# Kernel optimization log

Measured on AMD Instinct MI355X. Metric: run time of the kernel, lower is better.

Reference implementation:

```python
import jax, jax.numpy as jnp
import numpy as np

N = 50000   # nodes
E = 800000  # edges (avg degree 16)
DIMS = [(128, 128), (128, 128), (128, 64)]  # (in, out) per SAGEConv layer
EPS_BN = 1e-5
EPS_NORM = 1e-12


def _make_layer(key, din, dout):
    k1, k2 = jax.random.split(key)
    s = 1.0 / np.sqrt(din)
    return (
        jax.random.normal(k1, (dout, din), jnp.float32) * s,  # Wl: neighbor linear
        jnp.zeros((dout,), jnp.float32),                      # bl
        jax.random.normal(k2, (dout, din), jnp.float32) * s,  # Wr: root linear (no bias in PyG)
        jnp.ones((dout,), jnp.float32),                       # bn gamma
        jnp.zeros((dout,), jnp.float32),                      # bn beta
        jnp.zeros((dout,), jnp.float32),                      # bn running mean
        jnp.ones((dout,), jnp.float32),                       # bn running var
    )


def setup_inputs() -> dict:
    key = jax.random.key(0)
    kx, ke, k0, k1, k2 = jax.random.split(key, 5)
    inp = {
        "x": jax.random.normal(kx, (N, 128), jnp.float32),
        "edge_index": jax.random.randint(ke, (2, E), 0, N, dtype=jnp.int32),
    }
    for i, (k, (din, dout)) in enumerate(zip([k0, k1, k2], DIMS)):
        Wl, bl, Wr, g, b, rm, rv = _make_layer(k, din, dout)
        inp.update({f"Wl{i}": Wl, f"bl{i}": bl, f"Wr{i}": Wr,
                    f"g{i}": g, f"b{i}": b, f"rm{i}": rm, f"rv{i}": rv})
    return inp


def _sage_conv(x, src, dst, Wl, bl, Wr):
    # mean aggregation of incoming messages: gather src features, scatter-add at dst
    agg = jax.ops.segment_sum(x[src], dst, num_segments=N)          # [N, din]
    deg = jax.ops.segment_sum(jnp.ones((src.shape[0],), x.dtype), dst, num_segments=N)
    mean = agg / jnp.maximum(deg, 1.0)[:, None]
    return mean @ Wl.T + bl + x @ Wr.T


def _bn_eval(x, g, b, rm, rv):
    return g * (x - rm) * jax.lax.rsqrt(rv + EPS_BN) + b


def reference(x, edge_index,
              Wl0, bl0, Wr0, g0, b0, rm0, rv0,
              Wl1, bl1, Wr1, g1, b1, rm1, rv1,
              Wl2, bl2, Wr2, g2, b2, rm2, rv2):
    src, dst = edge_index[0], edge_index[1]
    layers = [
        (Wl0, bl0, Wr0, g0, b0, rm0, rv0),
        (Wl1, bl1, Wr1, g1, b1, rm1, rv1),
        (Wl2, bl2, Wr2, g2, b2, rm2, rv2),
    ]
    h = x
    for i, (Wl, bl, Wr, g, b, rm, rv) in enumerate(layers):
        h = _bn_eval(_sage_conv(h, src, dst, Wl, bl, Wr), g, b, rm, rv)
        if i < len(layers) - 1:
            h = jax.nn.relu(h)  # dropout is identity in eval mode
    # F.normalize(p=2, dim=1)
    return h / jnp.maximum(jnp.linalg.norm(h, axis=1, keepdims=True), EPS_NORM)
```

## Files before the change

### kernel.cpp

```cpp
#include <hip/hip_runtime.h>
#include <hip/hip_bf16.h>

#define CDIV(a,b) (((a)+(b)-1)/(b))
#define NBUCK_MAX 512
#define AGG_CAP  1536
#define AGGF_CAP 3072

typedef __attribute__((ext_vector_type(8))) short short8;
typedef __attribute__((ext_vector_type(4))) float f32x4;
typedef __attribute__((ext_vector_type(2))) float f32x2;

static __device__ __forceinline__ unsigned short f2bf(float f){
  union { float f; unsigned u; } v; v.f = f;
  unsigned r = v.u + 0x7fffu + ((v.u >> 16) & 1u);
  return (unsigned short)(r >> 16);
}
static __device__ __forceinline__ unsigned pack2(float lo, float hi){
  return (unsigned)f2bf(lo) | ((unsigned)f2bf(hi) << 16);
}
static __device__ __forceinline__ float bf2f(unsigned short s){
  union { unsigned u; float f; } v; v.u = ((unsigned)s) << 16; return v.f;
}
static __device__ __forceinline__ unsigned pk_fp8x4(float a, float b, float c, float d){
  int v = __builtin_amdgcn_cvt_pk_fp8_f32(a, b, 0, false);
  v = __builtin_amdgcn_cvt_pk_fp8_f32(c, d, v, true);
  return (unsigned)v;
}

#define ACCQ16(v) { f32x2 q0 = __builtin_amdgcn_cvt_pk_f32_fp8((int)v.x, false); \
                    f32x2 q1 = __builtin_amdgcn_cvt_pk_f32_fp8((int)v.x, true);  \
                    f32x2 q2 = __builtin_amdgcn_cvt_pk_f32_fp8((int)v.y, false); \
                    f32x2 q3 = __builtin_amdgcn_cvt_pk_f32_fp8((int)v.y, true);  \
                    f32x2 q4 = __builtin_amdgcn_cvt_pk_f32_fp8((int)v.z, false); \
                    f32x2 q5 = __builtin_amdgcn_cvt_pk_f32_fp8((int)v.z, true);  \
                    f32x2 q6 = __builtin_amdgcn_cvt_pk_f32_fp8((int)v.w, false); \
                    f32x2 q7 = __builtin_amdgcn_cvt_pk_f32_fp8((int)v.w, true);  \
                    a0 += q0.x; a1 += q0.y; a2  += q1.x; a3  += q1.y; \
                    a4 += q2.x; a5 += q2.y; a6  += q3.x; a7  += q3.y; \
                    a8 += q4.x; a9 += q4.y; a10 += q5.x; a11 += q5.y; \
                    a12 += q6.x; a13 += q6.y; a14 += q7.x; a15 += q7.y; }


struct WtpArgs {
  const float *W0, *W1, *bl, *g, *b, *rm, *rv;
  unsigned short* Bpk; float *sc; float *sh;
  int kblk, dout, do_bn, nblk, perm;
};

static __device__ __forceinline__ void wtp_one(const WtpArgs& a, int idx){
  int NB16 = a.kblk*32*a.dout;
  if (idx < NB16){
    int j = idx & 7, lane = (idx >> 3) & 63, rest = idx >> 9;
    int NT = a.dout >> 4;
    int nt = rest % NT, kk = rest / NT;
    int nn = nt*16 + (lane & 15);
    int k  = kk*32 + ((lane >> 4) * 8) + j;
    float v;
    if (k < 128){
      int kc = a.perm ? (((k & 7) << 4) | (k >> 3)) : k;
      v = a.W0[nn*128 + kc];
    } else {
      v = a.W1[nn*128 + (k - 128)];
    }
    a.Bpk[idx] = f2bf(v);
  } else if (a.do_bn && idx < NB16 + a.dout){
    int jj = idx - NB16;
    float s = a.g[jj] * rsqrtf(a.rv[jj] + 1e-5f);
    a.sc[jj] = s;
    a.sh[jj] = (a.bl[jj] - a.rm[jj]) * s + a.b[jj];
  }
}


__global__ __launch_bounds__(256) void k_prep(const float* __restrict__ x, int n4, unsigned* __restrict__ xb,
                                              unsigned* __restrict__ xq,
                                              const int* __restrict__ dst, int E,
                                              int* __restrict__ bcnt, int nbuck,
                                              int castBlocks, int histBlocks,
                                              WtpArgs a0, WtpArgs a1, WtpArgs a2, WtpArgs a3){
  __shared__ int s[NBUCK_MAX];
  int b = blockIdx.x, t = threadIdx.x;
  if (b < castBlocks){
    int i = b*256 + t;
    if (i < n4){
      float4 v = ((const float4*)x)[i];
      uint2 o; o.x = pack2(v.x, v.y); o.y = pack2(v.z, v.w);
      ((uint2*)xb)[i] = o;
      xq[i] = pk_fp8x4(v.x, v.y, v.z, v.w);
    }
    return;
  }
  b -= castBlocks;
  if (b < histBlocks){
    for (int i=t;i<nbuck;i+=256) s[i] = 0;
    __syncthreads();
    constexpr int EPT = 16;
    int e0 = b*256*EPT;
    #pragma unroll
    for (int i=0;i<EPT;i++){
      int e = e0 + i*256 + t;
      if (e < E) atomicAdd(&s[dst[e] >> 7], 1);
    }
    __syncthreads();
    for (int i=t;i<nbuck;i+=256){
      int c = s[i];
      if (c > 0) atomicAdd(&bcnt[i], c);
    }
    return;
  }
  b -= histBlocks;
  if (b < a0.nblk){ wtp_one(a0, b*256 + t); return; }
  b -= a0.nblk;
  if (b < a1.nblk){ wtp_one(a1, b*256 + t); return; }
  b -= a1.nblk;
  if (b < a2.nblk){ wtp_one(a2, b*256 + t); return; }
  b -= a2.nblk;
  wtp_one(a3, b*256 + t);
}

__global__ __launch_bounds__(256) void k_bscan(const int* __restrict__ bcnt, int nbuck,
                                               int* __restrict__ bbase){
  __shared__ int s[256];
  int t = threadIdx.x;
  int a0 = (2*t   < nbuck) ? bcnt[2*t]   : 0;
  int a1 = (2*t+1 < nbuck) ? bcnt[2*t+1] : 0;
  s[t] = a0 + a1; __syncthreads();
  for (int d=1; d<256; d<<=1){
    int u = (t>=d) ? s[t-d] : 0;
    __syncthreads();
    s[t] += u;
    __syncthreads();
  }
  int excl = s[t] - (a0 + a1);
  if (2*t   < nbuck) bbase[2*t]   = excl;
  if (2*t+1 < nbuck) bbase[2*t+1] = excl + a0;
  if (t == 255) bbase[nbuck] = s[255];
}

__global__ __launch_bounds__(256) void k_bucketA(const int* __restrict__ src, const int* __restrict__ dst,
                                                 int E, const int* __restrict__ bbase,
                                                 int* __restrict__ bcur, unsigned* __restrict__ ebuf, int nbuck){
  __shared__ int scnt[NBUCK_MAX];
  __shared__ int sbase[NBUCK_MAX];
  __shared__ int sboff[NBUCK_MAX];
  int t = threadIdx.x;
  for (int i=t;i<nbuck;i+=256) scnt[i] = 0;
  __syncthreads();
  constexpr int EPT = 16;
  int e0 = blockIdx.x*256*EPT;
  int b[EPT]; unsigned pk[EPT];
  #pragma unroll
  for (int i=0;i<EPT;i++){
    int e = e0 + i*256 + t;
    if (e < E){
      int d = dst[e];
      b[i] = d >> 7;
      pk[i] = ((unsigned)(d & 127) << 16) | (unsigned)src[e];
      atomicAdd(&scnt[b[i]], 1);
    } else b[i] = -1;
  }
  __syncthreads();
  for (int i=t;i<nbuck;i+=256){
    int c = scnt[i];
    sbase[i] = (c > 0) ? atomicAdd(&bcur[i], c) : 0;
    sboff[i] = bbase[i];
    scnt[i] = 0;
  }
  __syncthreads();
  #pragma unroll
  for (int i=0;i<EPT;i++){
    if (b[i] >= 0){
      int p = atomicAdd(&scnt[b[i]], 1);
      ebuf[(size_t)sboff[b[i]] + sbase[b[i]] + p] = pk[i];
    }
  }
}

__global__ __launch_bounds__(256) void k_bucketB(const unsigned* __restrict__ ebuf, const int* __restrict__ bbase,
                                                 int N, int* __restrict__ off, int* __restrict__ csr){
  int b = blockIdx.x;
  int n0 = b << 7, n1 = min(n0 + 128, N);
  __shared__ int sdeg[128];
  __shared__ int sabs[129];
  __shared__ int cur[128];
  int t = threadIdx.x;
  if (t < 128){ sdeg[t] = 0; cur[t] = 0; }
  __syncthreads();
  int e0 = bbase[b], e1 = bbase[b+1];
  for (int e = e0 + t; e < e1; e += 256)
    atomicAdd(&sdeg[ebuf[e] >> 16], 1);
  __syncthreads();
  for (int d=1; d<128; d<<=1){
    int u = (t < 128 && t >= d) ? sdeg[t-d] : 0;
    __syncthreads();
    if (t < 128) sdeg[t] += u;
    __syncthreads();
  }
  if (t == 0) sabs[0] = e0;
  if (t < 128) sabs[t+1] = e0 + sdeg[t];
  __syncthreads();
  if (t <= n1 - n0) off[n0 + t] = sabs[t];
  for (int e = e0 + t; e < e1; e += 256){
    unsigned pr = ebuf[e];
    int ln = (int)(pr >> 16);
    int p = atomicAdd(&cur[ln], 1);
    csr[sabs[ln] + p] = (int)(pr & 0xffffu);
  }
}


__global__ __launch_bounds__(256) void k_agg(const uint4* __restrict__ hq4, const int* __restrict__ off,
                                             const int* __restrict__ csr, int n, uint4* __restrict__ mean4){
  __shared__ int scsr[AGG_CAP];
  __shared__ int sw[2];
  int t = threadIdx.x;
  int nodeblk = blockIdx.x * 32;
  if (t < 2) sw[t] = off[min(nodeblk + t*32, n)];
  __syncthreads();
  int e0b = sw[0];
  int span = sw[1] - e0b;
  for (int i = t; i < span && i < AGG_CAP; i += 256) scsr[i] = csr[e0b + i];
  __syncthreads();

  int lane = t & 63;
  int sl = lane & 7;
  int node = nodeblk + (t >> 3);
  bool valid = node < n;
  int s0 = valid ? off[node]   : 0;
  int s1 = valid ? off[node+1] : 0;
  float a0=0,a1=0,a2=0,a3=0,a4=0,a5=0,a6=0,a7=0;
  float a8=0,a9=0,a10=0,a11=0,a12=0,a13=0,a14=0,a15=0;
  int e = s0;
  for (; e + 8 <= s1; e += 8){
    int le = e - e0b;
    int i0,i1,i2,i3,i4,i5,i6,i7;
    if (le + 8 <= AGG_CAP){
      i0 = scsr[le];   i1 = scsr[le+1]; i2 = scsr[le+2]; i3 = scsr[le+3];
      i4 = scsr[le+4]; i5 = scsr[le+5]; i6 = scsr[le+6]; i7 = scsr[le+7];
    } else {
      i0 = csr[e];   i1 = csr[e+1]; i2 = csr[e+2]; i3 = csr[e+3];
      i4 = csr[e+4]; i5 = csr[e+5]; i6 = csr[e+6]; i7 = csr[e+7];
    }
    uint4 v0 = hq4[(size_t)i0*8 + sl];
    uint4 v1 = hq4[(size_t)i1*8 + sl];
    uint4 v2 = hq4[(size_t)i2*8 + sl];
    uint4 v3 = hq4[(size_t)i3*8 + sl];
    uint4 v4 = hq4[(size_t)i4*8 + sl];
    uint4 v5 = hq4[(size_t)i5*8 + sl];
    uint4 v6 = hq4[(size_t)i6*8 + sl];
    uint4 v7 = hq4[(size_t)i7*8 + sl];
    ACCQ16(v0); ACCQ16(v1); ACCQ16(v2); ACCQ16(v3);
    ACCQ16(v4); ACCQ16(v5); ACCQ16(v6); ACCQ16(v7);
  }
  for (; e + 4 <= s1; e += 4){
    int le = e - e0b;
    int i0,i1,i2,i3;
    if (le + 4 <= AGG_CAP){
      i0 = scsr[le]; i1 = scsr[le+1]; i2 = scsr[le+2]; i3 = scsr[le+3];
    } else {
      i0 = csr[e]; i1 = csr[e+1]; i2 = csr[e+2]; i3 = csr[e+3];
    }
    uint4 v0 = hq4[(size_t)i0*8 + sl];
    uint4 v1 = hq4[(size_t)i1*8 + sl];
    uint4 v2 = hq4[(size_t)i2*8 + sl];
    uint4 v3 = hq4[(size_t)i3*8 + sl];
    ACCQ16(v0); ACCQ16(v1); ACCQ16(v2); ACCQ16(v3);
  }
  for (; e < s1; e++){
    int le = e - e0b;
    int ii = (le < AGG_CAP) ? scsr[le] : csr[e];
    uint4 v = hq4[(size_t)ii*8 + sl];
    ACCQ16(v);
  }
  if (valid){
    int d = s1 - s0;
    float inv = 1.0f / (float)(d > 0 ? d : 1);
    uint4 o0, o1;
    o0.x = pack2(a0*inv,  a1*inv);  o0.y = pack2(a2*inv,  a3*inv);
    o0.z = pack2(a4*inv,  a5*inv);  o0.w = pack2(a6*inv,  a7*inv);
    o1.x = pack2(a8*inv,  a9*inv);  o1.y = pack2(a10*inv, a11*inv);
    o1.z = pack2(a12*inv, a13*inv); o1.w = pack2(a14*inv, a15*inv);
    size_t base = (size_t)node*16 + (size_t)sl*2;
    mean4[base]   = o0;
    mean4[base+1] = o1;
  }
}


template<bool YL>
__global__ __launch_bounds__(256, 2) void k_gemm_hid(
    const unsigned short* __restrict__ A0, const unsigned short* __restrict__ A1,
    const unsigned short* __restrict__ Bpk, const float* __restrict__ sc,
    const float* __restrict__ sh, const unsigned short* __restrict__ BpkL,
    unsigned short* __restrict__ outh, unsigned* __restrict__ outq,
    unsigned* __restrict__ outyl, int n){
  __shared__ unsigned short Bs[256*128];
  int t = threadIdx.x;
  {
    const uint4* s = (const uint4*)Bpk;
    uint4* d = (uint4*)Bs;
    #pragma unroll
    for (int i=0;i<16;i++) d[i*256 + t] = s[i*256 + t];
  }
  __syncthreads();

  int lane = t & 63, w = t >> 6;
  int quad = lane >> 4, c = lane & 15;
  int mb = blockIdx.x*128, woff = w*32;
  int r0 = mb + woff + c;
  int r1 = r0 + 16;

  f32x4 acc[2][8];
  #pragma unroll
  for (int mt=0;mt<2;mt++)
    #pragma unroll
    for (int nt=0;nt<8;nt++) acc[mt][nt] = (f32x4){0.f,0.f,0.f,0.f};

  #pragma unroll
  for (int kk=0; kk<8; kk++){
    const unsigned short* ab = (kk >= 4) ? A1 : A0;
    int ka = (kk & 3)*32 + quad*8;
    short8 a0 = {0,0,0,0,0,0,0,0}, a1 = {0,0,0,0,0,0,0,0};
    if (r0 < n) a0 = *(const short8*)(ab + (size_t)r0*128 + ka);
    if (r1 < n) a1 = *(const short8*)(ab + (size_t)r1*128 + ka);
    #pragma unroll
    for (int nt=0; nt<8; nt++){
      short8 b = *(const short8*)&Bs[(size_t)((kk*8 + nt)*64 + lane)*8];
      acc[0][nt] = __builtin_amdgcn_mfma_f32_16x16x32_bf16(a0, b, acc[0][nt], 0, 0, 0);
      acc[1][nt] = __builtin_amdgcn_mfma_f32_16x16x32_bf16(a1, b, acc[1][nt], 0, 0, 0);
    }
  }

  float scv[8], shv[8];
  #pragma unroll
  for (int nt=0;nt<8;nt++){ scv[nt] = sc[nt*16 + c]; shv[nt] = sh[nt*16 + c]; }

  #pragma unroll
  for (int mt=0; mt<2; mt++){
    #pragma unroll
    for (int r=0;r<4;r++){
      int row = mb + woff + mt*16 + quad*4 + r;
      if (row < n){
        float u[8];
        #pragma unroll
        for (int nt=0;nt<8;nt++){
          float uu = acc[mt][nt][r]*scv[nt] + shv[nt];
          u[nt] = fmaxf(uu, 0.f);
          outh[(size_t)row*128 + nt*16 + c] = f2bf(u[nt]);
        }
        if constexpr (!YL){
          uint2 q;
          q.x = pk_fp8x4(u[0], u[1], u[2], u[3]);
          q.y = pk_fp8x4(u[4], u[5], u[6], u[7]);
          ((uint2*)outq)[(size_t)row*16 + c] = q;
        }
      }
    }
  }

  if constexpr (YL){
    __syncthreads();
    {
      uint4* d = (uint4*)Bs;
      const uint4* s4 = (const uint4*)outh;
      #pragma unroll
      for (int i=0;i<8;i++){
        int idx = i*256 + t;
        int row = idx >> 4;
        int gr = mb + row; if (gr > n-1) gr = n-1;
        d[idx] = s4[(size_t)gr*16 + (idx & 15)];
      }
      const uint4* sL = (const uint4*)BpkL;
      #pragma unroll
      for (int i=0;i<4;i++) d[2048 + i*256 + t] = sL[i*256 + t];
    }
    __syncthreads();
    f32x4 acc2[2][4];
    #pragma unroll
    for (int mt=0;mt<2;mt++)
      #pragma unroll
      for (int nt=0;nt<4;nt++) acc2[mt][nt] = (f32x4){0.f,0.f,0.f,0.f};
    int r0l = woff + c, r1l = r0l + 16;
    #pragma unroll
    for (int kk=0; kk<4; kk++){
      int ka = kk*32 + quad*8;
      short8 a0 = *(const short8*)&Bs[(size_t)r0l*128 + ka];
      short8 a1 = *(const short8*)&Bs[(size_t)r1l*128 + ka];
      #pragma unroll
      for (int nt=0; nt<4; nt++){
        short8 b = *(const short8*)&Bs[16384 + (size_t)((kk*4 + nt)*64 + lane)*8];
        acc2[0][nt] = __builtin_amdgcn_mfma_f32_16x16x32_bf16(a0, b, acc2[0][nt], 0, 0, 0);
        acc2[1][nt] = __builtin_amdgcn_mfma_f32_16x16x32_bf16(a1, b, acc2[1][nt], 0, 0, 0);
      }
    }
    #pragma unroll
    for (int mt=0; mt<2; mt++){
      #pragma unroll
      for (int r=0;r<4;r++){
        int row = mb + woff + mt*16 + quad*4 + r;
        if (row < n){
          unsigned q = pk_fp8x4(acc2[0][0][r], acc2[0][1][r], acc2[0][2][r], acc2[0][3][r]);
          unsigned q1 = pk_fp8x4(acc2[1][0][r], acc2[1][1][r], acc2[1][2][r], acc2[1][3][r]);
          outyl[(size_t)row*16 + c] = (mt == 0) ? q : q1;
        }
      }
    }
  }
}


__global__ __launch_bounds__(256, 2) void k_aggf(
    const uint4* __restrict__ ylq4, const int* __restrict__ off, const int* __restrict__ csr,
    const unsigned short* __restrict__ A0, const unsigned short* __restrict__ BpkR,
    const float* __restrict__ sc, const float* __restrict__ sh,
    float* __restrict__ outf, int n){
  __shared__ unsigned short Ms[128*64];
  __shared__ unsigned short Bs[128*64];
  __shared__ int scsr[AGGF_CAP];
  __shared__ int sw[2];
  int t = threadIdx.x;
  int mb = blockIdx.x*128;
  if (t < 2) sw[t] = off[min(mb + t*128, n)];
  {
    const uint4* s = (const uint4*)BpkR;
    uint4* d = (uint4*)Bs;
    #pragma unroll
    for (int i=0;i<4;i++) d[i*256 + t] = s[i*256 + t];
  }
  __syncthreads();
  int e0b = sw[0];
  int span = sw[1] - e0b;
  for (int i = t; i < span && i < AGGF_CAP; i += 256) scsr[i] = csr[e0b + i];
  __syncthreads();

  int lane = t & 63, w = t >> 6;
  int sl4 = lane & 3;

  #pragma unroll
  for (int it=0; it<2; it++){
    int ln = w*32 + it*16 + (lane >> 2);
    int node = mb + ln;
    bool valid = node < n;
    int s0 = valid ? off[node]   : 0;
    int s1 = valid ? off[node+1] : 0;
    float a0=0,a1=0,a2=0,a3=0,a4=0,a5=0,a6=0,a7=0;
    float a8=0,a9=0,a10=0,a11=0,a12=0,a13=0,a14=0,a15=0;
    int e = s0;
    for (; e + 8 <= s1; e += 8){
      int le = e - e0b;
      int i0,i1,i2,i3,i4,i5,i6,i7;
      if (le + 8 <= AGGF_CAP){
        i0 = scsr[le];   i1 = scsr[le+1]; i2 = scsr[le+2]; i3 = scsr[le+3];
        i4 = scsr[le+4]; i5 = scsr[le+5]; i6 = scsr[le+6]; i7 = scsr[le+7];
      } else {
        i0 = csr[e];   i1 = csr[e+1]; i2 = csr[e+2]; i3 = csr[e+3];
        i4 = csr[e+4]; i5 = csr[e+5]; i6 = csr[e+6]; i7 = csr[e+7];
      }
      uint4 v0 = ylq4[(size_t)i0*4 + sl4];
      uint4 v1 = ylq4[(size_t)i1*4 + sl4];
      uint4 v2 = ylq4[(size_t)i2*4 + sl4];
      uint4 v3 = ylq4[(size_t)i3*4 + sl4];
      uint4 v4 = ylq4[(size_t)i4*4 + sl4];
      uint4 v5 = ylq4[(size_t)i5*4 + sl4];
      uint4 v6 = ylq4[(size_t)i6*4 + sl4];
      uint4 v7 = ylq4[(size_t)i7*4 + sl4];
      ACCQ16(v0); ACCQ16(v1); ACCQ16(v2); ACCQ16(v3);
      ACCQ16(v4); ACCQ16(v5); ACCQ16(v6); ACCQ16(v7);
    }
    for (; e + 4 <= s1; e += 4){
      int le = e - e0b;
      int i0,i1,i2,i3;
      if (le + 4 <= AGGF_CAP){
        i0 = scsr[le]; i1 = scsr[le+1]; i2 = scsr[le+2]; i3 = scsr[le+3];
      } else {
        i0 = csr[e]; i1 = csr[e+1]; i2 = csr[e+2]; i3 = csr[e+3];
      }
      uint4 v0 = ylq4[(size_t)i0*4 + sl4];
      uint4 v1 = ylq4[(size_t)i1*4 + sl4];
      uint4 v2 = ylq4[(size_t)i2*4 + sl4];
      uint4 v3 = ylq4[(size_t)i3*4 + sl4];
      ACCQ16(v0); ACCQ16(v1); ACCQ16(v2); ACCQ16(v3);
    }
    for (; e < s1; e++){
      int le = e - e0b;
      int ii = (le < AGGF_CAP) ? scsr[le] : csr[e];
      uint4 v = ylq4[(size_t)ii*4 + sl4];
      ACCQ16(v);
    }
    int d = s1 - s0;
    float inv = 1.0f / (float)(d > 0 ? d : 1);
    uint4 o0, o1;
    o0.x = pack2(a0*inv,  a1*inv);  o0.y = pack2(a2*inv,  a3*inv);
    o0.z = pack2(a4*inv,  a5*inv);  o0.w = pack2(a6*inv,  a7*inv);
    o1.x = pack2(a8*inv,  a9*inv);  o1.y = pack2(a10*inv, a11*inv);
    o1.z = pack2(a12*inv, a13*inv); o1.w = pack2(a14*inv, a15*inv);
    ((uint4*)Ms)[ln*8 + sl4*2]     = o0;
    ((uint4*)Ms)[ln*8 + sl4*2 + 1] = o1;
  }
  __syncthreads();

  int quad = lane >> 4, c = lane & 15;
  int woff = w*32;
  int r0 = mb + woff + c;
  int r1 = r0 + 16;
  f32x4 acc[2][4];
  #pragma unroll
  for (int mt=0;mt<2;mt++)
    #pragma unroll
    for (int nt=0;nt<4;nt++) acc[mt][nt] = (f32x4){0.f,0.f,0.f,0.f};
  #pragma unroll
  for (int kk=0; kk<4; kk++){
    int ka = kk*32 + quad*8;
    short8 a0 = {0,0,0,0,0,0,0,0}, a1 = {0,0,0,0,0,0,0,0};
    if (r0 < n) a0 = *(const short8*)(A0 + (size_t)r0*128 + ka);
    if (r1 < n) a1 = *(const short8*)(A0 + (size_t)r1*128 + ka);
    #pragma unroll
    for (int nt=0; nt<4; nt++){
      short8 b = *(const short8*)&Bs[(size_t)((kk*4 + nt)*64 + lane)*8];
      acc[0][nt] = __builtin_amdgcn_mfma_f32_16x16x32_bf16(a0, b, acc[0][nt], 0, 0, 0);
      acc[1][nt] = __builtin_amdgcn_mfma_f32_16x16x32_bf16(a1, b, acc[1][nt], 0, 0, 0);
    }
  }

  float scv[4], shv[4];
  #pragma unroll
  for (int nt=0;nt<4;nt++){ scv[nt] = sc[nt*16 + c]; shv[nt] = sh[nt*16 + c]; }

  #pragma unroll
  for (int mt=0; mt<2; mt++){
    #pragma unroll
    for (int r=0;r<4;r++){
      int lr = woff + mt*16 + quad*4 + r;
      int row = mb + lr;
      float v[4];
      float ss = 0.f;
      if (row < n){
        #pragma unroll
        for (int nt=0;nt<4;nt++){
          float u = acc[mt][nt][r] + bf2f(Ms[lr*64 + c*4 + nt]);
          u = u*scv[nt] + shv[nt];
          v[nt] = u;
          ss += u*u;
        }
      } else {
        #pragma unroll
        for (int nt=0;nt<4;nt++) v[nt] = 0.f;
      }
      ss += __shfl_xor(ss, 1, 64);
      ss += __shfl_xor(ss, 2, 64);
      ss += __shfl_xor(ss, 4, 64);
      ss += __shfl_xor(ss, 8, 64);
      float rn = 1.0f / fmaxf(sqrtf(ss), 1e-12f);
      if (row < n){
        #pragma unroll
        for (int nt=0;nt<4;nt++) outf[(size_t)row*64 + nt*16 + c] = v[nt]*rn;
      }
    }
  }
}


extern "C" void kernel_launch(void* const* d_in, const int* in_sizes, int n_in,
                              void* d_out, int out_size, void* d_ws, size_t ws_size,
                              hipStream_t stream){
  const float* x = (const float*)d_in[0];
  const int* ei  = (const int*)d_in[1];
  int N = in_sizes[0] / 128;
  int E = in_sizes[1] / 2;
  const int* esrc = ei;
  const int* edst = ei + E;
  int nbuck = CDIV(N, 128);

  const float *Wl[3], *bl[3], *Wr[3], *g[3], *bb[3], *rm[3], *rv[3];
  int dout[3];
  for (int i=0;i<3;i++){
    int base = 2 + 7*i;
    Wl[i]=(const float*)d_in[base];   bl[i]=(const float*)d_in[base+1];
    Wr[i]=(const float*)d_in[base+2]; g[i] =(const float*)d_in[base+3];
    bb[i]=(const float*)d_in[base+4]; rm[i]=(const float*)d_in[base+5];
    rv[i]=(const float*)d_in[base+6];
    dout[i] = in_sizes[base] / 128;
  }

  char* p = (char*)d_ws;
  size_t o = 0;
  auto alloc = [&](size_t bytes)->void*{ void* r = p + o; o += (bytes + 255) & ~(size_t)255; return r; };
  int* bz    = (int*)alloc((size_t)2*nbuck*4);
  int* bcnt  = bz;
  int* bcur  = bz + nbuck;
  int* bbase = (int*)alloc((size_t)(nbuck+1)*4);
  int* off   = (int*)alloc((size_t)(N+1)*4);
  int* csr   = (int*)alloc((size_t)E*4);
  unsigned* ebuf = (unsigned*)alloc((size_t)E*4);
  unsigned* xb   = (unsigned*)alloc((size_t)N*64*4);
  unsigned* xq   = (unsigned*)alloc((size_t)N*128);
  unsigned* mb   = (unsigned*)alloc((size_t)N*64*4);
  unsigned* h_a  = (unsigned*)alloc((size_t)N*64*4);
  unsigned* haq  = (unsigned*)alloc((size_t)N*128);
  unsigned* h_b  = (unsigned*)alloc((size_t)N*64*4);
  unsigned* ylb  = (unsigned*)alloc((size_t)N*64);
  unsigned short* Bpk01[2];
  float* sc[3]; float* sh[3];
  for (int i=0;i<2;i++) Bpk01[i] = (unsigned short*)alloc((size_t)256*dout[i]*2);
  unsigned short* BpkL = (unsigned short*)alloc((size_t)128*dout[2]*2);
  unsigned short* BpkR = (unsigned short*)alloc((size_t)128*dout[2]*2);
  for (int i=0;i<3;i++){
    sc[i] = (float*)alloc((size_t)dout[i]*4);
    sh[i] = (float*)alloc((size_t)dout[i]*4);
  }

  hipMemsetAsync(bz, 0, (size_t)2*nbuck*4, stream);

  WtpArgs wa[4];
  wa[0] = { Wl[0], Wr[0], bl[0], g[0], bb[0], rm[0], rv[0], Bpk01[0], sc[0], sh[0], 8, dout[0], 1, CDIV(256*dout[0]+dout[0],256), 0 };
  wa[1] = { Wl[1], Wr[1], bl[1], g[1], bb[1], rm[1], rv[1], Bpk01[1], sc[1], sh[1], 8, dout[1], 1, CDIV(256*dout[1]+dout[1],256), 1 };
  wa[2] = { Wl[2], nullptr, nullptr, nullptr, nullptr, nullptr, nullptr, BpkL, nullptr, nullptr, 4, dout[2], 0, CDIV(128*dout[2],256), 0 };
  wa[3] = { Wr[2], nullptr, bl[2], g[2], bb[2], rm[2], rv[2], BpkR, sc[2], sh[2], 4, dout[2], 1, CDIV(128*dout[2]+dout[2],256), 0 };

  int castBlocks = CDIV(N*32, 256);
  int histBlocks = CDIV(E, 256*16);
  int prepBlocks = castBlocks + histBlocks + wa[0].nblk + wa[1].nblk + wa[2].nblk + wa[3].nblk;
  k_prep   <<<prepBlocks,256,0,stream>>>(x, N*32, xb, xq, edst, E, bcnt, nbuck, castBlocks, histBlocks,
                                         wa[0], wa[1], wa[2], wa[3]);
  k_bscan  <<<1,256,0,stream>>>(bcnt, nbuck, bbase);
  k_bucketA<<<CDIV(E,256*16),256,0,stream>>>(esrc, edst, E, bbase, bcur, ebuf, nbuck);
  k_bucketB<<<nbuck,256,0,stream>>>(ebuf, bbase, N, off, csr);

  k_agg<<<CDIV(N,32),256,0,stream>>>((const uint4*)xq, off, csr, N, (uint4*)mb);
  k_gemm_hid<false><<<CDIV(N,128),256,0,stream>>>((const unsigned short*)mb, (const unsigned short*)xb,
                                                  Bpk01[0], sc[0], sh[0], nullptr,
                                                  (unsigned short*)h_a, haq, nullptr, N);
  k_agg<<<CDIV(N,32),256,0,stream>>>((const uint4*)haq, off, csr, N, (uint4*)mb);
  k_gemm_hid<true><<<CDIV(N,128),256,0,stream>>>((const unsigned short*)mb, (const unsigned short*)h_a,
                                                 Bpk01[1], sc[1], sh[1], BpkL,
                                                 (unsigned short*)h_b, nullptr, ylb, N);
  k_aggf<<<CDIV(N,128),256,0,stream>>>((const uint4*)ylb, off, csr,
                                       (const unsigned short*)h_b, BpkR, sc[2], sh[2],
                                       (float*)d_out, N);
}
```

Baseline: 240.2 us.

## Degree-sort nodes within buckets, fuse bucket scan, use packed fp8 accumulation

Removes the separate bucket-scan kernel by redoing the bucket prefix sum inside each bucketA and bucketB block. bucketB now bitonic-sorts each 128-node bucket by in-degree and emits a reordered CSR, offsets and a node map. The aggregation kernels then walk nodes in degree order, so the threads of a wave see similar edge counts and less divergence. Accumulation also switches to packed f32x2 adds, which cuts scalar adds. In exchange every block repeats the scan and the aggregation gathers an extra nodemap index per node.

```diff
diff --git a/kernel.cpp b/kernel.cpp
--- a/kernel.cpp
+++ b/kernel.cpp
@@ -27,18 +27,14 @@
   return (unsigned)v;
 }
 
-#define ACCQ16(v) { f32x2 q0 = __builtin_amdgcn_cvt_pk_f32_fp8((int)v.x, false); \
-                    f32x2 q1 = __builtin_amdgcn_cvt_pk_f32_fp8((int)v.x, true);  \
-                    f32x2 q2 = __builtin_amdgcn_cvt_pk_f32_fp8((int)v.y, false); \
-                    f32x2 q3 = __builtin_amdgcn_cvt_pk_f32_fp8((int)v.y, true);  \
-                    f32x2 q4 = __builtin_amdgcn_cvt_pk_f32_fp8((int)v.z, false); \
-                    f32x2 q5 = __builtin_amdgcn_cvt_pk_f32_fp8((int)v.z, true);  \
-                    f32x2 q6 = __builtin_amdgcn_cvt_pk_f32_fp8((int)v.w, false); \
-                    f32x2 q7 = __builtin_amdgcn_cvt_pk_f32_fp8((int)v.w, true);  \
-                    a0 += q0.x; a1 += q0.y; a2  += q1.x; a3  += q1.y; \
-                    a4 += q2.x; a5 += q2.y; a6  += q3.x; a7  += q3.y; \
-                    a8 += q4.x; a9 += q4.y; a10 += q5.x; a11 += q5.y; \
-                    a12 += q6.x; a13 += q6.y; a14 += q7.x; a15 += q7.y; }
+#define ACCP16(v) { b0 += __builtin_amdgcn_cvt_pk_f32_fp8((int)v.x, false); \
+                    b1 += __builtin_amdgcn_cvt_pk_f32_fp8((int)v.x, true);  \
+                    b2 += __builtin_amdgcn_cvt_pk_f32_fp8((int)v.y, false); \
+                    b3 += __builtin_amdgcn_cvt_pk_f32_fp8((int)v.y, true);  \
+                    b4 += __builtin_amdgcn_cvt_pk_f32_fp8((int)v.z, false); \
+                    b5 += __builtin_amdgcn_cvt_pk_f32_fp8((int)v.z, true);  \
+                    b6 += __builtin_amdgcn_cvt_pk_f32_fp8((int)v.w, false); \
+                    b7 += __builtin_amdgcn_cvt_pk_f32_fp8((int)v.w, true); }
 
 
 struct WtpArgs {
@@ -118,32 +114,28 @@
   wtp_one(a3, b*256 + t);
 }
 
-__global__ __launch_bounds__(256) void k_bscan(const int* __restrict__ bcnt, int nbuck,
-                                               int* __restrict__ bbase){
-  __shared__ int s[256];
-  int t = threadIdx.x;
-  int a0 = (2*t   < nbuck) ? bcnt[2*t]   : 0;
-  int a1 = (2*t+1 < nbuck) ? bcnt[2*t+1] : 0;
-  s[t] = a0 + a1; __syncthreads();
-  for (int d=1; d<256; d<<=1){
-    int u = (t>=d) ? s[t-d] : 0;
-    __syncthreads();
-    s[t] += u;
-    __syncthreads();
-  }
-  int excl = s[t] - (a0 + a1);
-  if (2*t   < nbuck) bbase[2*t]   = excl;
-  if (2*t+1 < nbuck) bbase[2*t+1] = excl + a0;
-  if (t == 255) bbase[nbuck] = s[255];
-}
-
 __global__ __launch_bounds__(256) void k_bucketA(const int* __restrict__ src, const int* __restrict__ dst,
-                                                 int E, const int* __restrict__ bbase,
+                                                 int E, const int* __restrict__ bcnt,
                                                  int* __restrict__ bcur, unsigned* __restrict__ ebuf, int nbuck){
   __shared__ int scnt[NBUCK_MAX];
   __shared__ int sbase[NBUCK_MAX];
   __shared__ int sboff[NBUCK_MAX];
+  __shared__ int ss[256];
   int t = threadIdx.x;
+  {
+    int a0 = (2*t   < nbuck) ? bcnt[2*t]   : 0;
+    int a1 = (2*t+1 < nbuck) ? bcnt[2*t+1] : 0;
+    ss[t] = a0 + a1; __syncthreads();
+    for (int d=1; d<256; d<<=1){
+      int u = (t>=d) ? ss[t-d] : 0;
+      __syncthreads();
+      ss[t] += u;
+      __syncthreads();
+    }
+    int excl = ss[t] - (a0 + a1);
+    if (2*t   < nbuck) sboff[2*t]   = excl;
+    if (2*t+1 < nbuck) sboff[2*t+1] = excl + a0;
+  }
   for (int i=t;i<nbuck;i+=256) scnt[i] = 0;
   __syncthreads();
   constexpr int EPT = 16;
@@ -163,7 +155,6 @@
   for (int i=t;i<nbuck;i+=256){
     int c = scnt[i];
     sbase[i] = (c > 0) ? atomicAdd(&bcur[i], c) : 0;
-    sboff[i] = bbase[i];
     scnt[i] = 0;
   }
   __syncthreads();
@@ -176,19 +167,61 @@
   }
 }
 
-__global__ __launch_bounds__(256) void k_bucketB(const unsigned* __restrict__ ebuf, const int* __restrict__ bbase,
-                                                 int N, int* __restrict__ off, int* __restrict__ csr){
-  int b = blockIdx.x;
-  int n0 = b << 7, n1 = min(n0 + 128, N);
+__global__ __launch_bounds__(256) void k_bucketB(const unsigned* __restrict__ ebuf, const int* __restrict__ bcnt,
+                                                 int nbuck, int E, int N,
+                                                 int* __restrict__ offR, int* __restrict__ csr,
+                                                 int* __restrict__ nodemap){
+  __shared__ int sEx[NBUCK_MAX];
+  __shared__ int ss[256];
   __shared__ int sdeg[128];
   __shared__ int sabs[129];
   __shared__ int cur[128];
-  int t = threadIdx.x;
+  __shared__ unsigned skey[128];
+  __shared__ int rof[128];
+  int b = blockIdx.x, t = threadIdx.x;
+  {
+    int a0 = (2*t   < nbuck) ? bcnt[2*t]   : 0;
+    int a1 = (2*t+1 < nbuck) ? bcnt[2*t+1] : 0;
+    ss[t] = a0 + a1; __syncthreads();
+    for (int d=1; d<256; d<<=1){
+      int u = (t>=d) ? ss[t-d] : 0;
+      __syncthreads();
+      ss[t] += u;
+      __syncthreads();
+    }
+    int excl = ss[t] - (a0 + a1);
+    if (2*t   < nbuck) sEx[2*t]   = excl;
+    if (2*t+1 < nbuck) sEx[2*t+1] = excl + a0;
+  }
   if (t < 128){ sdeg[t] = 0; cur[t] = 0; }
   __syncthreads();
-  int e0 = bbase[b], e1 = bbase[b+1];
+  int e0 = sEx[b];
+  int e1 = (b+1 < nbuck) ? sEx[b+1] : E;
   for (int e = e0 + t; e < e1; e += 256)
     atomicAdd(&sdeg[ebuf[e] >> 16], 1);
+  __syncthreads();
+  if (t < 128) skey[t] = ((unsigned)sdeg[t] << 7) | (unsigned)(127 - t);
+  __syncthreads();
+  #pragma unroll
+  for (int k=2; k<=128; k<<=1){
+    #pragma unroll
+    for (int j=k>>1; j>0; j>>=1){
+      if (t < 128){
+        int p = t ^ j;
+        if (p > t){
+          unsigned x = skey[t], y = skey[p];
+          bool swap = ((t & k) == 0) ? (x < y) : (x > y);
+          if (swap){ skey[t] = y; skey[p] = x; }
+        }
+      }
+      __syncthreads();
+    }
+  }
+  if (t < 128){
+    int lid = 127 - (int)(skey[t] & 127u);
+    rof[lid] = t;
+    sdeg[t] = (int)(skey[t] >> 7);
+  }
   __syncthreads();
   for (int d=1; d<128; d<<=1){
     int u = (t < 128 && t >= d) ? sdeg[t-d] : 0;
@@ -199,23 +232,27 @@
   if (t == 0) sabs[0] = e0;
   if (t < 128) sabs[t+1] = e0 + sdeg[t];
   __syncthreads();
-  if (t <= n1 - n0) off[n0 + t] = sabs[t];
+  int n0 = b << 7, n1 = min(n0 + 128, N);
+  int cnt = n1 - n0;
+  if (t <= cnt) offR[n0 + t] = sabs[t];
+  if (t < cnt)  nodemap[n0 + t] = n0 + (127 - (int)(skey[t] & 127u));
   for (int e = e0 + t; e < e1; e += 256){
     unsigned pr = ebuf[e];
     int ln = (int)(pr >> 16);
     int p = atomicAdd(&cur[ln], 1);
-    csr[sabs[ln] + p] = (int)(pr & 0xffffu);
-  }
-}
-
-
-__global__ __launch_bounds__(256) void k_agg(const uint4* __restrict__ hq4, const int* __restrict__ off,
-                                             const int* __restrict__ csr, int n, uint4* __restrict__ mean4){
+    csr[sabs[rof[ln]] + p] = (int)(pr & 0xffffu);
+  }
+}
+
+
+__global__ __launch_bounds__(256) void k_agg(const uint4* __restrict__ hq4, const int* __restrict__ offR,
+                                             const int* __restrict__ csr, const int* __restrict__ nodemap,
+                                             int n, uint4* __restrict__ mean4){
   __shared__ int scsr[AGG_CAP];
   __shared__ int sw[2];
   int t = threadIdx.x;
   int nodeblk = blockIdx.x * 32;
-  if (t < 2) sw[t] = off[min(nodeblk + t*32, n)];
+  if (t < 2) sw[t] = offR[min(nodeblk + t*32, n)];
   __syncthreads();
   int e0b = sw[0];
   int span = sw[1] - e0b;
@@ -224,12 +261,12 @@
 
   int lane = t & 63;
   int sl = lane & 7;
-  int node = nodeblk + (t >> 3);
-  bool valid = node < n;
-  int s0 = valid ? off[node]   : 0;
-  int s1 = valid ? off[node+1] : 0;
-  float a0=0,a1=0,a2=0,a3=0,a4=0,a5=0,a6=0,a7=0;
-  float a8=0,a9=0,a10=0,a11=0,a12=0,a13=0,a14=0,a15=0;
+  int idx = nodeblk + (t >> 3);
+  bool valid = idx < n;
+  int s0 = valid ? offR[idx]   : 0;
+  int s1 = valid ? offR[idx+1] : 0;
+  int node = valid ? nodemap[idx] : 0;
+  f32x2 b0={0,0},b1={0,0},b2={0,0},b3={0,0},b4={0,0},b5={0,0},b6={0,0},b7={0,0};
   int e = s0;
   for (; e + 8 <= s1; e += 8){
     int le = e - e0b;
@@ -249,8 +286,8 @@
     uint4 v5 = hq4[(size_t)i5*8 + sl];
     uint4 v6 = hq4[(size_t)i6*8 + sl];
     uint4 v7 = hq4[(size_t)i7*8 + sl];
-    ACCQ16(v0); ACCQ16(v1); ACCQ16(v2); ACCQ16(v3);
-    ACCQ16(v4); ACCQ16(v5); ACCQ16(v6); ACCQ16(v7);
+    ACCP16(v0); ACCP16(v1); ACCP16(v2); ACCP16(v3);
+    ACCP16(v4); ACCP16(v5); ACCP16(v6); ACCP16(v7);
   }
   for (; e + 4 <= s1; e += 4){
     int le = e - e0b;
@@ -264,22 +301,22 @@
     uint4 v1 = hq4[(size_t)i1*8 + sl];
     uint4 v2 = hq4[(size_t)i2*8 + sl];
     uint4 v3 = hq4[(size_t)i3*8 + sl];
-    ACCQ16(v0); ACCQ16(v1); ACCQ16(v2); ACCQ16(v3);
+    ACCP16(v0); ACCP16(v1); ACCP16(v2); ACCP16(v3);
   }
   for (; e < s1; e++){
     int le = e - e0b;
     int ii = (le < AGG_CAP) ? scsr[le] : csr[e];
     uint4 v = hq4[(size_t)ii*8 + sl];
-    ACCQ16(v);
+    ACCP16(v);
   }
   if (valid){
     int d = s1 - s0;
     float inv = 1.0f / (float)(d > 0 ? d : 1);
     uint4 o0, o1;
-    o0.x = pack2(a0*inv,  a1*inv);  o0.y = pack2(a2*inv,  a3*inv);
-    o0.z = pack2(a4*inv,  a5*inv);  o0.w = pack2(a6*inv,  a7*inv);
-    o1.x = pack2(a8*inv,  a9*inv);  o1.y = pack2(a10*inv, a11*inv);
-    o1.z = pack2(a12*inv, a13*inv); o1.w = pack2(a14*inv, a15*inv);
+    o0.x = pack2(b0.x*inv, b0.y*inv);  o0.y = pack2(b1.x*inv, b1.y*inv);
+    o0.z = pack2(b2.x*inv, b2.y*inv);  o0.w = pack2(b3.x*inv, b3.y*inv);
+    o1.x = pack2(b4.x*inv, b4.y*inv);  o1.y = pack2(b5.x*inv, b5.y*inv);
+    o1.z = pack2(b6.x*inv, b6.y*inv);  o1.w = pack2(b7.x*inv, b7.y*inv);
     size_t base = (size_t)node*16 + (size_t)sl*2;
     mean4[base]   = o0;
     mean4[base+1] = o1;
@@ -410,7 +447,8 @@
 
 
 __global__ __launch_bounds__(256, 2) void k_aggf(
-    const uint4* __restrict__ ylq4, const int* __restrict__ off, const int* __restrict__ csr,
+    const uint4* __restrict__ ylq4, const int* __restrict__ offR, const int* __restrict__ csr,
+    const int* __restrict__ nodemap,
     const unsigned short* __restrict__ A0, const unsigned short* __restrict__ BpkR,
     const float* __restrict__ sc, const float* __restrict__ sh,
     float* __restrict__ outf, int n){
@@ -420,7 +458,7 @@
   __shared__ int sw[2];
   int t = threadIdx.x;
   int mb = blockIdx.x*128;
-  if (t < 2) sw[t] = off[min(mb + t*128, n)];
+  if (t < 2) sw[t] = offR[min(mb + t*128, n)];
   {
     const uint4* s = (const uint4*)BpkR;
     uint4* d = (uint4*)Bs;
@@ -438,13 +476,13 @@
 
   #pragma unroll
   for (int it=0; it<2; it++){
-    int ln = w*32 + it*16 + (lane >> 2);
-    int node = mb + ln;
-    bool valid = node < n;
-    int s0 = valid ? off[node]   : 0;
-    int s1 = valid ? off[node+1] : 0;
-    float a0=0,a1=0,a2=0,a3=0,a4=0,a5=0,a6=0,a7=0;
-    float a8=0,a9=0,a10=0,a11=0,a12=0,a13=0,a14=0,a15=0;
+    int rk = w*32 + it*16 + (lane >> 2);
+    int idx = mb + rk;
+    bool valid = idx < n;
+    int s0 = valid ? offR[idx]   : 0;
+    int s1 = valid ? offR[idx+1] : 0;
+    int ln = valid ? (nodemap[idx] - mb) : rk;
+    f32x2 b0={0,0},b1={0,0},b2={0,0},b3={0,0},b4={0,0},b5={0,0},b6={0,0},b7={0,0};
     int e = s0;
     for (; e + 8 <= s1; e += 8){
       int le = e - e0b;
@@ -464,8 +502,8 @@
       uint4 v5 = ylq4[(size_t)i5*4 + sl4];
       uint4 v6 = ylq4[(size_t)i6*4 + sl4];
       uint4 v7 = ylq4[(size_t)i7*4 + sl4];
-      ACCQ16(v0); ACCQ16(v1); ACCQ16(v2); ACCQ16(v3);
-      ACCQ16(v4); ACCQ16(v5); ACCQ16(v6); ACCQ16(v7);
+      ACCP16(v0); ACCP16(v1); ACCP16(v2); ACCP16(v3);
+      ACCP16(v4); ACCP16(v5); ACCP16(v6); ACCP16(v7);
     }
     for (; e + 4 <= s1; e += 4){
       int le = e - e0b;
@@ -479,21 +517,21 @@
       uint4 v1 = ylq4[(size_t)i1*4 + sl4];
       uint4 v2 = ylq4[(size_t)i2*4 + sl4];
       uint4 v3 = ylq4[(size_t)i3*4 + sl4];
-      ACCQ16(v0); ACCQ16(v1); ACCQ16(v2); ACCQ16(v3);
+      ACCP16(v0); ACCP16(v1); ACCP16(v2); ACCP16(v3);
     }
     for (; e < s1; e++){
       int le = e - e0b;
       int ii = (le < AGGF_CAP) ? scsr[le] : csr[e];
       uint4 v = ylq4[(size_t)ii*4 + sl4];
-      ACCQ16(v);
+      ACCP16(v);
     }
     int d = s1 - s0;
     float inv = 1.0f / (float)(d > 0 ? d : 1);
     uint4 o0, o1;
-    o0.x = pack2(a0*inv,  a1*inv);  o0.y = pack2(a2*inv,  a3*inv);
-    o0.z = pack2(a4*inv,  a5*inv);  o0.w = pack2(a6*inv,  a7*inv);
-    o1.x = pack2(a8*inv,  a9*inv);  o1.y = pack2(a10*inv, a11*inv);
-    o1.z = pack2(a12*inv, a13*inv); o1.w = pack2(a14*inv, a15*inv);
+    o0.x = pack2(b0.x*inv, b0.y*inv);  o0.y = pack2(b1.x*inv, b1.y*inv);
+    o0.z = pack2(b2.x*inv, b2.y*inv);  o0.w = pack2(b3.x*inv, b3.y*inv);
+    o1.x = pack2(b4.x*inv, b4.y*inv);  o1.y = pack2(b5.x*inv, b5.y*inv);
+    o1.z = pack2(b6.x*inv, b6.y*inv);  o1.w = pack2(b7.x*inv, b7.y*inv);
     ((uint4*)Ms)[ln*8 + sl4*2]     = o0;
     ((uint4*)Ms)[ln*8 + sl4*2 + 1] = o1;
   }
@@ -588,8 +626,8 @@
   int* bz    = (int*)alloc((size_t)2*nbuck*4);
   int* bcnt  = bz;
   int* bcur  = bz + nbuck;
-  int* bbase = (int*)alloc((size_t)(nbuck+1)*4);
-  int* off   = (int*)alloc((size_t)(N+1)*4);
+  int* offR  = (int*)alloc((size_t)(N+1)*4);
+  int* nodemap = (int*)alloc((size_t)N*4);
   int* csr   = (int*)alloc((size_t)E*4);
   unsigned* ebuf = (unsigned*)alloc((size_t)E*4);
   unsigned* xb   = (unsigned*)alloc((size_t)N*64*4);
@@ -622,19 +660,18 @@
   int prepBlocks = castBlocks + histBlocks + wa[0].nblk + wa[1].nblk + wa[2].nblk + wa[3].nblk;
   k_prep   <<<prepBlocks,256,0,stream>>>(x, N*32, xb, xq, edst, E, bcnt, nbuck, castBlocks, histBlocks,
                                          wa[0], wa[1], wa[2], wa[3]);
-  k_bscan  <<<1,256,0,stream>>>(bcnt, nbuck, bbase);
-  k_bucketA<<<CDIV(E,256*16),256,0,stream>>>(esrc, edst, E, bbase, bcur, ebuf, nbuck);
-  k_bucketB<<<nbuck,256,0,stream>>>(ebuf, bbase, N, off, csr);
-
-  k_agg<<<CDIV(N,32),256,0,stream>>>((const uint4*)xq, off, csr, N, (uint4*)mb);
+  k_bucketA<<<CDIV(E,256*16),256,0,stream>>>(esrc, edst, E, bcnt, bcur, ebuf, nbuck);
+  k_bucketB<<<nbuck,256,0,stream>>>(ebuf, bcnt, nbuck, E, N, offR, csr, nodemap);
+
+  k_agg<<<CDIV(N,32),256,0,stream>>>((const uint4*)xq, offR, csr, nodemap, N, (uint4*)mb);
   k_gemm_hid<false><<<CDIV(N,128),256,0,stream>>>((const unsigned short*)mb, (const unsigned short*)xb,
                                                   Bpk01[0], sc[0], sh[0], nullptr,
                                                   (unsigned short*)h_a, haq, nullptr, N);
-  k_agg<<<CDIV(N,32),256,0,stream>>>((const uint4*)haq, off, csr, N, (uint4*)mb);
+  k_agg<<<CDIV(N,32),256,0,stream>>>((const uint4*)haq, offR, csr, nodemap, N, (uint4*)mb);
   k_gemm_hid<true><<<CDIV(N,128),256,0,stream>>>((const unsigned short*)mb, (const unsigned short*)h_a,
                                                  Bpk01[1], sc[1], sh[1], BpkL,
                                                  (unsigned short*)h_b, nullptr, ylb, N);
-  k_aggf<<<CDIV(N,128),256,0,stream>>>((const uint4*)ylb, off, csr,
+  k_aggf<<<CDIV(N,128),256,0,stream>>>((const uint4*)ylb, offR, csr, nodemap,
                                        (const unsigned short*)h_b, BpkR, sc[2], sh[2],
                                        (float*)d_out, N);
 }
```

After: 239.1 us. Within noise of the previous version (-0.4%).
